# Optimization experiments

Hardware: AMD Instinct MI355X
Metric: run time of the kernel (lower is better)

The kernel has to match this reference:

```python
import jax, jax.numpy as jnp
import numpy as np

B, N, K, H, F_IN = 16, 2048, 8, 128, 4  # graphs, nodes/graph, knn k, hidden, input feats


def _lin(key, fi, fo):
    s = 1.0 / np.sqrt(fi)
    kw, kb = jax.random.split(key)
    W = jax.random.uniform(kw, (fi, fo), jnp.float32, -s, s)
    b = jax.random.uniform(kb, (fo,), jnp.float32, -s, s)
    return W, b


def setup_inputs() -> dict:
    key = jax.random.key(0)
    ks = jax.random.split(key, 10)
    x = jax.random.normal(ks[0], (B * N, F_IN), jnp.float32)
    edge_index = jax.random.randint(ks[1], (2, B * N * K), 0, B * N, jnp.int64)  # unused by forward
    batch = jnp.repeat(jnp.arange(B, dtype=jnp.int64), N)
    W_enc, b_enc = _lin(ks[2], F_IN, H)
    W1a, b1a = _lin(ks[3], 2 * H, H)
    W1b, b1b = _lin(ks[4], H, H)
    W2a, b2a = _lin(ks[5], 2 * H, H)
    W2b, b2b = _lin(ks[6], H, H)
    W5a, b5a = _lin(ks[7], 2 * H, H)
    W5b, b5b = _lin(ks[8], H, 1)
    return dict(x=x, edge_index=edge_index, batch=batch,
                W_enc=W_enc, b_enc=b_enc,
                W1a=W1a, b1a=b1a, W1b=W1b, b1b=b1b,
                W2a=W2a, b2a=b2a, W2b=W2b, b2b=b2b,
                W5a=W5a, b5a=b5a, W5b=W5b, b5b=b5b)


def _knn(xb):
    # xb: [N, H] -> [N, K] indices of k nearest neighbors (self included, as in torch_cluster.knn)
    sq = jnp.sum(xb * xb, axis=-1)
    d = sq[:, None] + sq[None, :] - 2.0 * (xb @ xb.T)  # squared distances [N, N]
    return jax.lax.top_k(-d, K)[1]


def _edge_conv(x, Wa, ba, Wb, bb):
    # DynamicEdgeConv: rebuild kNN on current features, message = MLP([x_i, x_j - x_i]), max-aggregate.
    idx = jax.vmap(_knn)(x)                                   # [B, N, K]
    xj = jax.vmap(lambda xb, ib: xb[ib])(x, idx)              # [B, N, K, Hin]
    xi = jnp.broadcast_to(x[:, :, None, :], xj.shape)
    e = jnp.concatenate([xi, xj - xi], axis=-1)               # [B, N, K, 2*Hin]
    h = jax.nn.relu(e @ Wa + ba)                              # MLP applies ReLU after each Linear
    h = jax.nn.relu(h @ Wb + bb)
    return jnp.max(h, axis=2)                                 # max aggregation over neighbors


def reference(x, edge_index, batch, W_enc, b_enc,
              W1a, b1a, W1b, b1b, W2a, b2a, W2b, b2b, W5a, b5a, W5b, b5b):
    # batch is contiguous equal-size graphs -> reshape; edge_index is ignored by the original forward.
    h = x.reshape(B, N, F_IN) @ W_enc + b_enc
    h = jax.nn.relu(_edge_conv(h, W1a, b1a, W1b, b1b))
    h = jax.nn.relu(_edge_conv(h, W2a, b2a, W2b, b2b))
    out = jax.nn.sigmoid(_edge_conv(h, W5a, b5a, W5b, b5b))   # note: last MLP layer also has ReLU
    return out.reshape(B * N, 1)
```

## Files before the change

### kernel.cpp

```cpp
#include <hip/hip_runtime.h>
#include <hip/hip_bf16.h>
#include <math.h>

#define BGR 16
#define NPG 2048
#define HD  128
#define KNN 8
#define NTOT (BGR*NPG)

using bf16x8 = __attribute__((ext_vector_type(8))) short;
using f32x4  = __attribute__((ext_vector_type(4))) float;
using f32x16 = __attribute__((ext_vector_type(16))) float;

typedef __attribute__((address_space(3))) unsigned int lds_uint;
typedef const __attribute__((address_space(1))) unsigned int glob_uint;
#define GLOAD_LDS16(g, l) __builtin_amdgcn_global_load_lds((glob_uint*)(g), (lds_uint*)(l), 16, 0, 0)

__device__ inline unsigned short bf16rn(float f) {
    unsigned u = __float_as_uint(f);
    unsigned r = (u + 0x7FFFu + ((u >> 16) & 1u)) >> 16;
    return (unsigned short)r;
}
__device__ inline float bf16tof(unsigned short h) {
    return __uint_as_float(((unsigned)h) << 16);
}

__global__ __launch_bounds__(256) void enc_split(const float* __restrict__ x,
                                                 const float* __restrict__ W,
                                                 const float* __restrict__ bias,
                                                 unsigned short* __restrict__ hs,
                                                 float* __restrict__ sqg)
{
    const size_t plane = (size_t)NTOT * HD;
    int node = (blockIdx.x * 256 + threadIdx.x) >> 6;
    int lane = threadIdx.x & 63;
    float4 xv = *(const float4*)(x + (size_t)node * 4);
    float v0 = bias[lane], v1 = bias[lane + 64];
    const float* xf = (const float*)&xv;
#pragma unroll
    for (int f = 0; f < 4; ++f) {
        v0 = fmaf(xf[f], W[f * 128 + lane], v0);
        v1 = fmaf(xf[f], W[f * 128 + lane + 64], v1);
    }
    float s = fmaf(v0, v0, v1 * v1);
#pragma unroll
    for (int off = 32; off >= 1; off >>= 1)
        s += __shfl_xor(s, off);
    if (lane == 0) sqg[node] = s;
#pragma unroll
    for (int q = 0; q < 2; ++q) {
        float v = q ? v1 : v0;
        int   d = lane + q * 64;
        unsigned short b1 = bf16rn(v);  float r1 = v - bf16tof(b1);
        unsigned short b2 = bf16rn(r1);
        size_t base = (size_t)node * HD + d;
        hs[base]         = b1;
        hs[base + plane] = b2;
    }
}

__global__ __launch_bounds__(256) void prep_wcat(const float* __restrict__ Wa,
                                                 unsigned short* __restrict__ Wt)
{
    int gid = blockIdx.x * 256 + threadIdx.x;
    int k = gid >> 8, n = gid & 255;
    float w;
    if (n < 128) w = Wa[(128 + k) * 128 + n];
    else { int nn = n - 128; w = Wa[k * 128 + nn] - Wa[(128 + k) * 128 + nn]; }
    unsigned short b1 = bf16rn(w);  float r1 = w - bf16tof(b1);
    unsigned short b2 = bf16rn(r1);
    int cs = n >> 5, h = (n >> 4) & 1, c = n & 15, kc = k >> 5, kg = (k >> 3) & 3, e = k & 7;
    size_t off = (size_t)cs * 12288 + kc * 1024 + h * 512 + kg * 128 + c * 8 + e;
    Wt[off] = b1; Wt[off + 4096] = b2;
}

__global__ __launch_bounds__(256) void prep_wb(const float* __restrict__ Wb,
                                               unsigned short* __restrict__ Wt)
{
    int gid = blockIdx.x * 256 + threadIdx.x;
    int k = gid >> 7, n = gid & 127;
    float w = Wb[k * 128 + n];
    unsigned short b1 = bf16rn(w);  float r1 = w - bf16tof(b1);
    unsigned short b2 = bf16rn(r1);
    int cs = n >> 5, h = (n >> 4) & 1, c = n & 15, kc = k >> 5, kg = (k >> 3) & 3, e = k & 7;
    size_t off = (size_t)cs * 12288 + kc * 1024 + h * 512 + kg * 128 + c * 8 + e;
    Wt[off] = b1; Wt[off + 4096] = b2;
}

#define THREEPASS(B00,B01,B10,B11) \
    acc0 = __builtin_amdgcn_mfma_f32_16x16x32_bf16(A0[kc], B00, acc0, 0, 0, 0); \
    acc1 = __builtin_amdgcn_mfma_f32_16x16x32_bf16(A0[kc], B01, acc1, 0, 0, 0); \
    acc0 = __builtin_amdgcn_mfma_f32_16x16x32_bf16(A1[kc], B00, acc0, 0, 0, 0); \
    acc1 = __builtin_amdgcn_mfma_f32_16x16x32_bf16(A1[kc], B01, acc1, 0, 0, 0); \
    acc0 = __builtin_amdgcn_mfma_f32_16x16x32_bf16(A0[kc], B10, acc0, 0, 0, 0); \
    acc1 = __builtin_amdgcn_mfma_f32_16x16x32_bf16(A0[kc], B11, acc1, 0, 0, 0);

#define SELECT(PACC, PS) { \
    const unsigned lidbase = (unsigned)((PS) << 4); \
    _Pragma("unroll") \
    for (int grp = 0; grp < 4; ++grp) { \
        f32x4 sq4 = *(const f32x4*)(sqs + (PS) * 32 + grp * 8 + kh * 4); \
        _Pragma("unroll") \
        for (int e = 0; e < 4; ++e) { \
            float dp = (sqi + sq4[e]) + (PACC)[grp * 4 + e]; \
            unsigned ku = (__float_as_uint(dp) & 0xFFFFFF00u) \
                        | (lidbase + (unsigned)(grp * 4 + e)); \
            float kk = __uint_as_float(ku); \
            bd[7] = __builtin_amdgcn_fmed3f(bd[6], kk, bd[7]); \
            bd[6] = __builtin_amdgcn_fmed3f(bd[5], kk, bd[6]); \
            bd[5] = __builtin_amdgcn_fmed3f(bd[4], kk, bd[5]); \
            bd[4] = __builtin_amdgcn_fmed3f(bd[3], kk, bd[4]); \
            bd[3] = __builtin_amdgcn_fmed3f(bd[2], kk, bd[3]); \
            bd[2] = __builtin_amdgcn_fmed3f(bd[1], kk, bd[2]); \
            bd[1] = __builtin_amdgcn_fmed3f(bd[0], kk, bd[1]); \
            bd[0] = fminf(bd[0], kk); \
        } \
    } }

__global__ __launch_bounds__(256, 3) void knn_mfma(const unsigned short* __restrict__ hs,
                                                   const float* __restrict__ sqg,
                                                   float* __restrict__ cand_d,
                                                   int* __restrict__ cand_i)
{
    __shared__ ulong2 ldsraw[2176];
    char* ldsc = (char*)ldsraw;
    float* sqs = (float*)(ldsc + 32768);

    const size_t plane = (size_t)NTOT * HD;
    const int t = threadIdx.x;
    const int b = blockIdx.x;
    const int slot = b >> 3;
    const int g  = (b & 7) | ((slot & 1) << 3);
    const int rb = (slot >> 1) & 15;
    const int cs = (slot >> 5) & 3;
    const int gbase = g * NPG;
    const int cbase = cs * 512;
    const int wv = t >> 6, lane = t & 63;
    const int rl = lane & 31, kh = lane >> 5;
    const int myrow = rb * 128 + wv * 32 + rl;

    sqs[t]       = sqg[gbase + cbase + t];
    sqs[t + 256] = sqg[gbase + cbase + 256 + t];

    bf16x8 RB[2][8];
    {
        const unsigned short* rrow = hs + (size_t)(gbase + myrow) * HD + kh * 8;
#pragma unroll
        for (int p = 0; p < 2; ++p)
#pragma unroll
            for (int kch = 0; kch < 8; ++kch) {
                bf16x8 v = *(const bf16x8*)(rrow + (size_t)p * plane + kch * 16);
                unsigned* u = (unsigned*)&v;
#pragma unroll
                for (int w = 0; w < 4; ++w)
                    u[w] = (u[w] + 0x00800080u) ^ 0x80008000u;
                RB[p][kch] = v;
            }
    }
    const float sqi = sqg[gbase + myrow];

    const unsigned short* sb = hs + (size_t)(gbase + cbase + (t & 31)) * HD
                             + (t >> 6) * 16 + ((t >> 5) & 1) * 8;
    char* ldsw = ldsc + wv * 1024;

#pragma unroll
    for (int i = 0; i < 4; ++i)
        GLOAD_LDS16(sb + (size_t)(i >> 1) * plane + (i & 1) * 64, ldsw + i * 4096);
    __syncthreads();

    const float INF = __uint_as_float(0x7F800000u);
    float bd[8];
#pragma unroll
    for (int s = 0; s < 8; ++s) bd[s] = INF;

    f32x16 pacc;
    int cur = 0;
    for (int s = 0; s < 16; ++s) {
        if (s < 15) {
            const unsigned short* sbn = sb + (size_t)(s + 1) * 32 * HD;
#pragma unroll
            for (int i = 0; i < 4; ++i)
                GLOAD_LDS16(sbn + (size_t)(i >> 1) * plane + (i & 1) * 64,
                            ldsw + (cur ^ 1) * 16384 + i * 4096);
        }
        const char* pstep = ldsc + cur * 16384 + lane * 16;
        f32x16 acc = {0.f,0.f,0.f,0.f,0.f,0.f,0.f,0.f,0.f,0.f,0.f,0.f,0.f,0.f,0.f,0.f};
        __builtin_amdgcn_s_setprio(1);
#pragma unroll
        for (int kch = 0; kch < 8; ++kch) {
            bf16x8 c0 = *(const bf16x8*)(pstep + kch * 1024);
            bf16x8 c1 = *(const bf16x8*)(pstep + 8192 + kch * 1024);
            acc = __builtin_amdgcn_mfma_f32_32x32x16_bf16(c0, RB[0][kch], acc, 0, 0, 0);
            acc = __builtin_amdgcn_mfma_f32_32x32x16_bf16(c1, RB[0][kch], acc, 0, 0, 0);
            acc = __builtin_amdgcn_mfma_f32_32x32x16_bf16(c0, RB[1][kch], acc, 0, 0, 0);
        }
        __builtin_amdgcn_s_setprio(0);
        if (s > 0) SELECT(pacc, s - 1)
        pacc = acc;
        __syncthreads();
        cur ^= 1;
    }
    SELECT(pacc, 15)

    const size_t ob = (size_t)(gbase + myrow) * 64 + cs * 16 + kh * 8;
#pragma unroll
    for (int sel = 0; sel < 8; ++sel) {
        unsigned u = __float_as_uint(bd[sel]);
        unsigned lid = u & 255u;
        int j = cbase + (int)(lid >> 4) * 32 + (int)((lid >> 2) & 3u) * 8
              + kh * 4 + (int)(lid & 3u);
        cand_d[ob + sel] = bd[sel];
        cand_i[ob + sel] = gbase + j;
    }
}

__global__ __launch_bounds__(256) void knn_merge(const float* __restrict__ cand_d,
                                                 const int* __restrict__ cand_i,
                                                 int* __restrict__ nbr)
{
    const int t = threadIdx.x;
    const int row = blockIdx.x * 32 + (t >> 3);
    const int run = t & 7;
    const float* pd = cand_d + (size_t)row * 64 + run * 8;
    const int*   pi = cand_i + (size_t)row * 64 + run * 8;
    float d[8]; int ix[8];
#pragma unroll
    for (int k = 0; k < 8; ++k) { d[k] = pd[k]; ix[k] = pi[k]; }
    const float INF = __uint_as_float(0x7F800000u);
    int* op = nbr + (size_t)row * KNN;
    float hd = d[0]; int hi = ix[0];
#pragma unroll
    for (int sel = 0; sel < 8; ++sel) {
        float md = hd; int mi = hi;
#pragma unroll
        for (int m = 1; m < 8; m <<= 1) {
            float od = __shfl_xor(md, m, 8);
            int   oi = __shfl_xor(mi, m, 8);
            bool tk = (od < md) || (od == md && oi < mi);
            md = tk ? od : md; mi = tk ? oi : mi;
        }
        if (run == sel) op[sel] = mi;
        bool win = (hd == md) && (hi == mi);
        if (win) {
            d[0]=d[1]; ix[0]=ix[1]; d[1]=d[2]; ix[1]=ix[2];
            d[2]=d[3]; ix[2]=ix[3]; d[3]=d[4]; ix[3]=ix[4];
            d[4]=d[5]; ix[4]=ix[5]; d[5]=d[6]; ix[5]=ix[6];
            d[6]=d[7]; ix[6]=ix[7]; d[7]=INF;  ix[7]=0x7fffffff;
        }
        hd = d[0]; hi = ix[0];
    }
}

__global__ __launch_bounds__(256) void node_gemm(const unsigned short* __restrict__ hs,
                                                 const unsigned short* __restrict__ Wt,
                                                 const float* __restrict__ ba,
                                                 float* __restrict__ P,
                                                 float* __restrict__ D)
{
    __shared__ char lds[32768];
    const size_t plane = (size_t)NTOT * HD;
    const int t = threadIdx.x, wv = t >> 6, lane = t & 63;
    const int lrow = lane & 15, kg = lane >> 4;
    const int nodebase = blockIdx.x * 64 + wv * 16;

    const unsigned short* arow = hs + (size_t)(nodebase + lrow) * HD + kg * 8;
    bf16x8 A0[4], A1[4];
#pragma unroll
    for (int kc = 0; kc < 4; ++kc) {
        A0[kc] = *(const bf16x8*)(arow + kc * 32);
        A1[kc] = *(const bf16x8*)(arow + plane + kc * 32);
    }

    char* ldsw = lds + wv * 1024;
    const unsigned short* wsrc = Wt + t * 8;
#pragma unroll
    for (int i = 0; i < 4; ++i)
        GLOAD_LDS16(wsrc + i * 2048, ldsw + i * 4096);
    __syncthreads();

    int cur = 0;
    for (int cs = 0; cs < 8; ++cs) {
        if (cs < 7) {
#pragma unroll
            for (int i = 0; i < 4; ++i)
                GLOAD_LDS16(wsrc + (size_t)(cs + 1) * 12288 + i * 2048,
                            ldsw + (cur ^ 1) * 16384 + i * 4096);
        }
        const char* pb = lds + cur * 16384 + kg * 256 + lrow * 16;
        f32x4 acc0 = {0.f,0.f,0.f,0.f};
        f32x4 acc1 = {0.f,0.f,0.f,0.f};
#pragma unroll
        for (int kc = 0; kc < 4; ++kc) {
            const char* pk = pb + kc * 2048;
            bf16x8 b00 = *(const bf16x8*)(pk);
            bf16x8 b01 = *(const bf16x8*)(pk + 1024);
            bf16x8 b10 = *(const bf16x8*)(pk + 8192);
            bf16x8 b11 = *(const bf16x8*)(pk + 9216);
            THREEPASS(b00, b01, b10, b11)
        }
        int n0 = cs * 32 + lrow;
        if (cs < 4) {
#pragma unroll
            for (int r = 0; r < 4; ++r) {
                size_t row = (size_t)(nodebase + kg * 4 + r) * HD;
                P[row + n0]      = acc0[r];
                P[row + n0 + 16] = acc1[r];
            }
        } else {
            float ba0 = ba[n0 - 128], ba1 = ba[n0 - 112];
#pragma unroll
            for (int r = 0; r < 4; ++r) {
                size_t row = (size_t)(nodebase + kg * 4 + r) * HD;
                D[row + n0 - 128] = acc0[r] + ba0;
                D[row + n0 - 112] = acc1[r] + ba1;
            }
        }
        __syncthreads();
        cur ^= 1;
    }
}

template<bool FINAL>
__global__ __launch_bounds__(256) void edge_mlp(const float* __restrict__ P,
                                                const float* __restrict__ D,
                                                const int* __restrict__ nbr,
                                                const unsigned short* __restrict__ Wbt,
                                                const float* __restrict__ bb,
                                                const float* __restrict__ w5,
                                                unsigned short* __restrict__ hsout,
                                                float* __restrict__ sqgout,
                                                float* __restrict__ out)
{
    __shared__ char lds[32768];
    const size_t plane = (size_t)NTOT * HD;
    const int t = threadIdx.x, wv = t >> 6, lane = t & 63;
    const int lrow = lane & 15, kg = lane >> 4;
    const int nodeA = blockIdx.x * 8 + wv * 2;
    const int i_node = nodeA + (lrow >> 3);
    const int j = nbr[(size_t)i_node * KNN + (lrow & 7)];

    const float* dp = D + (size_t)i_node * HD + kg * 8;
    const float* pp = P + (size_t)j * HD + kg * 8;

    bf16x8 A0[4], A1[4];
    float sdot = 0.f;
#pragma unroll
    for (int kc = 0; kc < 4; ++kc) {
        float4 d0 = *(const float4*)(dp + kc * 32);
        float4 d1 = *(const float4*)(dp + kc * 32 + 4);
        float4 p0 = *(const float4*)(pp + kc * 32);
        float4 p1 = *(const float4*)(pp + kc * 32 + 4);
        float v[8];
        v[0]=fmaxf(d0.x+p0.x,0.f); v[1]=fmaxf(d0.y+p0.y,0.f);
        v[2]=fmaxf(d0.z+p0.z,0.f); v[3]=fmaxf(d0.w+p0.w,0.f);
        v[4]=fmaxf(d1.x+p1.x,0.f); v[5]=fmaxf(d1.y+p1.y,0.f);
        v[6]=fmaxf(d1.z+p1.z,0.f); v[7]=fmaxf(d1.w+p1.w,0.f);
        if (FINAL) {
#pragma unroll
            for (int e = 0; e < 8; ++e)
                sdot = fmaf(v[e], w5[kc * 32 + kg * 8 + e], sdot);
        } else {
#pragma unroll
            for (int e = 0; e < 8; ++e) {
                unsigned short b1 = bf16rn(v[e]); float r1 = v[e] - bf16tof(b1);
                unsigned short b2 = bf16rn(r1);
                A0[kc][e] = (short)b1; A1[kc][e] = (short)b2;
            }
        }
    }

    if (!FINAL) {
        char* ldsw = lds + wv * 1024;
        const unsigned short* wsrc = Wbt + t * 8;
#pragma unroll
        for (int i = 0; i < 4; ++i)
            GLOAD_LDS16(wsrc + i * 2048, ldsw + i * 4096);
        __syncthreads();

        const int mynode = nodeA + (kg >> 1);
        const bool writer = (kg & 1) == 0;
        float sqacc = 0.f;

        int cur = 0;
        for (int cs = 0; cs < 4; ++cs) {
            if (cs < 3) {
#pragma unroll
                for (int i = 0; i < 4; ++i)
                    GLOAD_LDS16(wsrc + (size_t)(cs + 1) * 12288 + i * 2048,
                                ldsw + (cur ^ 1) * 16384 + i * 4096);
            }
            const char* pb = lds + cur * 16384 + kg * 256 + lrow * 16;
            f32x4 acc0 = {0.f,0.f,0.f,0.f};
            f32x4 acc1 = {0.f,0.f,0.f,0.f};
#pragma unroll
            for (int kc = 0; kc < 4; ++kc) {
                const char* pk = pb + kc * 2048;
                bf16x8 b00 = *(const bf16x8*)(pk);
                bf16x8 b01 = *(const bf16x8*)(pk + 1024);
                bf16x8 b10 = *(const bf16x8*)(pk + 8192);
                bf16x8 b11 = *(const bf16x8*)(pk + 9216);
                THREEPASS(b00, b01, b10, b11)
            }
            float bb0 = bb[cs * 32 + lrow];
            float bb1 = bb[cs * 32 + 16 + lrow];
            float m0 = fmaxf(fmaxf(acc0[0], acc0[1]), fmaxf(acc0[2], acc0[3]));
            float m1 = fmaxf(fmaxf(acc1[0], acc1[1]), fmaxf(acc1[2], acc1[3]));
            m0 = fmaxf(m0 + bb0, 0.f);
            m1 = fmaxf(m1 + bb1, 0.f);
            m0 = fmaxf(m0, __shfl_xor(m0, 16));
            m1 = fmaxf(m1, __shfl_xor(m1, 16));
            if (writer) {
                sqacc = fmaf(m0, m0, fmaf(m1, m1, sqacc));
                size_t base = (size_t)mynode * HD + cs * 32 + lrow;
                unsigned short c1 = bf16rn(m0); float r1 = m0 - bf16tof(c1);
                unsigned short c2 = bf16rn(r1);
                hsout[base]         = c1;
                hsout[base + plane] = c2;
                unsigned short e1 = bf16rn(m1); float s1 = m1 - bf16tof(e1);
                unsigned short e2 = bf16rn(s1);
                hsout[base + 16]         = e1;
                hsout[base + 16 + plane] = e2;
            }
            __syncthreads();
            cur ^= 1;
        }
        if (writer) {
#pragma unroll
            for (int m = 1; m < 16; m <<= 1)
                sqacc += __shfl_xor(sqacc, m, 16);
            if (lrow == 0) sqgout[mynode] = sqacc;
        }
    } else {
        sdot += __shfl_xor(sdot, 16);
        sdot += __shfl_xor(sdot, 32);
        float s = fmaxf(sdot + bb[0], 0.f);
#pragma unroll
        for (int m = 1; m < 8; m <<= 1)
            s = fmaxf(s, __shfl_xor(s, m));
        if (lane == 0) out[nodeA]     = 1.f / (1.f + expf(-s));
        if (lane == 8) out[nodeA + 1] = 1.f / (1.f + expf(-s));
    }
}

extern "C" void kernel_launch(void* const* d_in, const int* in_sizes, int n_in,
                              void* d_out, int out_size, void* d_ws, size_t ws_size,
                              hipStream_t stream) {
    const float* x     = (const float*)d_in[0];
    const float* W_enc = (const float*)d_in[3];
    const float* b_enc = (const float*)d_in[4];
    const float* W1a = (const float*)d_in[5];
    const float* b1a = (const float*)d_in[6];
    const float* W1b = (const float*)d_in[7];
    const float* b1b = (const float*)d_in[8];
    const float* W2a = (const float*)d_in[9];
    const float* b2a = (const float*)d_in[10];
    const float* W2b = (const float*)d_in[11];
    const float* b2b = (const float*)d_in[12];
    const float* W5a = (const float*)d_in[13];
    const float* b5a = (const float*)d_in[14];
    const float* W5b = (const float*)d_in[15];
    const float* b5b = (const float*)d_in[16];

    unsigned short* hs = (unsigned short*)d_ws;
    float* sqg  = (float*)(hs + (size_t)2*NTOT*HD);
    int*   idxb = (int*)(sqg + NTOT);
    float* Dbuf = (float*)(idxb + (size_t)NTOT*KNN);
    float* Pbuf = Dbuf + (size_t)NTOT*HD;
    unsigned short* Wt1  = (unsigned short*)(Pbuf + (size_t)NTOT*HD);
    unsigned short* Wt2  = Wt1 + 98304;
    unsigned short* Wt5  = Wt2 + 98304;
    unsigned short* Wbt1 = Wt5 + 98304;
    unsigned short* Wbt2 = Wbt1 + 49152;

    float* cd = Dbuf;
    int*   ci = (int*)(Dbuf + (size_t)NTOT*64);

    prep_wcat<<<128, 256, 0, stream>>>(W1a, Wt1);
    prep_wcat<<<128, 256, 0, stream>>>(W2a, Wt2);
    prep_wcat<<<128, 256, 0, stream>>>(W5a, Wt5);
    prep_wb  <<< 64, 256, 0, stream>>>(W1b, Wbt1);
    prep_wb  <<< 64, 256, 0, stream>>>(W2b, Wbt2);

    enc_split<<<NTOT/4, 256, 0, stream>>>(x, W_enc, b_enc, hs, sqg);

    knn_mfma   <<<1024, 256, 0, stream>>>(hs, sqg, cd, ci);
    knn_merge  <<<NTOT/32, 256, 0, stream>>>(cd, ci, idxb);
    node_gemm  <<<NTOT/64, 256, 0, stream>>>(hs, Wt1, b1a, Pbuf, Dbuf);
    edge_mlp<false><<<NTOT/8, 256, 0, stream>>>(Pbuf, Dbuf, idxb, Wbt1, b1b, nullptr, hs, sqg, nullptr);

    knn_mfma   <<<1024, 256, 0, stream>>>(hs, sqg, cd, ci);
    knn_merge  <<<NTOT/32, 256, 0, stream>>>(cd, ci, idxb);
    node_gemm  <<<NTOT/64, 256, 0, stream>>>(hs, Wt2, b2a, Pbuf, Dbuf);
    edge_mlp<false><<<NTOT/8, 256, 0, stream>>>(Pbuf, Dbuf, idxb, Wbt2, b2b, nullptr, hs, sqg, nullptr);

    knn_mfma   <<<1024, 256, 0, stream>>>(hs, sqg, cd, ci);
    knn_merge  <<<NTOT/32, 256, 0, stream>>>(cd, ci, idxb);
    node_gemm  <<<NTOT/64, 256, 0, stream>>>(hs, Wt5, b5a, Pbuf, Dbuf);
    edge_mlp<true><<<NTOT/8, 256, 0, stream>>>(Pbuf, Dbuf, idxb, nullptr, b5b, W5b, nullptr, nullptr, (float*)d_out);
}
```

Measured before the change: 372.1 us.

## Fuse setup kernels, merge kNN with node GEMM, fold merge into edge MLP

Combines the encoder and all weight-prep kernels into one launch. Runs the node GEMM as extra blocks in the same launch as the kNN MFMA kernel, since both read the same features. Moves the top-k candidate merge into the start of the edge MLP kernel, with the neighbour list kept in LDS, and issues the weight prefetch earlier. The kNN loop is unrolled by two with separate accumulators so SELECT overlaps the next MFMA step. Together this cuts six launches per layer pass plus the idx buffer round trip, at the cost of more complex blocks and a separate workspace for candidates.

```diff
diff --git a/kernel.cpp b/kernel.cpp
--- a/kernel.cpp
+++ b/kernel.cpp
@@ -25,44 +25,10 @@
     return __uint_as_float(((unsigned)h) << 16);
 }
 
-__global__ __launch_bounds__(256) void enc_split(const float* __restrict__ x,
-                                                 const float* __restrict__ W,
-                                                 const float* __restrict__ bias,
-                                                 unsigned short* __restrict__ hs,
-                                                 float* __restrict__ sqg)
+__device__ inline void wcat_body(const float* __restrict__ Wa,
+                                 unsigned short* __restrict__ Wt, int lb, int t)
 {
-    const size_t plane = (size_t)NTOT * HD;
-    int node = (blockIdx.x * 256 + threadIdx.x) >> 6;
-    int lane = threadIdx.x & 63;
-    float4 xv = *(const float4*)(x + (size_t)node * 4);
-    float v0 = bias[lane], v1 = bias[lane + 64];
-    const float* xf = (const float*)&xv;
-#pragma unroll
-    for (int f = 0; f < 4; ++f) {
-        v0 = fmaf(xf[f], W[f * 128 + lane], v0);
-        v1 = fmaf(xf[f], W[f * 128 + lane + 64], v1);
-    }
-    float s = fmaf(v0, v0, v1 * v1);
-#pragma unroll
-    for (int off = 32; off >= 1; off >>= 1)
-        s += __shfl_xor(s, off);
-    if (lane == 0) sqg[node] = s;
-#pragma unroll
-    for (int q = 0; q < 2; ++q) {
-        float v = q ? v1 : v0;
-        int   d = lane + q * 64;
-        unsigned short b1 = bf16rn(v);  float r1 = v - bf16tof(b1);
-        unsigned short b2 = bf16rn(r1);
-        size_t base = (size_t)node * HD + d;
-        hs[base]         = b1;
-        hs[base + plane] = b2;
-    }
-}
-
-__global__ __launch_bounds__(256) void prep_wcat(const float* __restrict__ Wa,
-                                                 unsigned short* __restrict__ Wt)
-{
-    int gid = blockIdx.x * 256 + threadIdx.x;
+    int gid = lb * 256 + t;
     int k = gid >> 8, n = gid & 255;
     float w;
     if (n < 128) w = Wa[(128 + k) * 128 + n];
@@ -74,10 +40,10 @@
     Wt[off] = b1; Wt[off + 4096] = b2;
 }
 
-__global__ __launch_bounds__(256) void prep_wb(const float* __restrict__ Wb,
-                                               unsigned short* __restrict__ Wt)
+__device__ inline void wb_body(const float* __restrict__ Wb,
+                               unsigned short* __restrict__ Wt, int lb, int t)
 {
-    int gid = blockIdx.x * 256 + threadIdx.x;
+    int gid = lb * 256 + t;
     int k = gid >> 7, n = gid & 127;
     float w = Wb[k * 128 + n];
     unsigned short b1 = bf16rn(w);  float r1 = w - bf16tof(b1);
@@ -85,6 +51,58 @@
     int cs = n >> 5, h = (n >> 4) & 1, c = n & 15, kc = k >> 5, kg = (k >> 3) & 3, e = k & 7;
     size_t off = (size_t)cs * 12288 + kc * 1024 + h * 512 + kg * 128 + c * 8 + e;
     Wt[off] = b1; Wt[off + 4096] = b2;
+}
+
+__global__ __launch_bounds__(256) void setup_all(const float* __restrict__ x,
+                                                 const float* __restrict__ We,
+                                                 const float* __restrict__ be,
+                                                 unsigned short* __restrict__ hs,
+                                                 float* __restrict__ sqg,
+                                                 const float* __restrict__ W1a,
+                                                 const float* __restrict__ W2a,
+                                                 const float* __restrict__ W5a,
+                                                 const float* __restrict__ W1b,
+                                                 const float* __restrict__ W2b,
+                                                 unsigned short* __restrict__ Wt1,
+                                                 unsigned short* __restrict__ Wt2,
+                                                 unsigned short* __restrict__ Wt5,
+                                                 unsigned short* __restrict__ Wbt1,
+                                                 unsigned short* __restrict__ Wbt2)
+{
+    const int bb = blockIdx.x, t = threadIdx.x;
+    if (bb < 8192) {
+        const size_t plane = (size_t)NTOT * HD;
+        int node = (bb * 256 + t) >> 6;
+        int lane = t & 63;
+        float4 xv = *(const float4*)(x + (size_t)node * 4);
+        float v0 = be[lane], v1 = be[lane + 64];
+        const float* xf = (const float*)&xv;
+#pragma unroll
+        for (int f = 0; f < 4; ++f) {
+            v0 = fmaf(xf[f], We[f * 128 + lane], v0);
+            v1 = fmaf(xf[f], We[f * 128 + lane + 64], v1);
+        }
+        float s = fmaf(v0, v0, v1 * v1);
+#pragma unroll
+        for (int off = 32; off >= 1; off >>= 1)
+            s += __shfl_xor(s, off);
+        if (lane == 0) sqg[node] = s;
+#pragma unroll
+        for (int q = 0; q < 2; ++q) {
+            float v = q ? v1 : v0;
+            int   d = lane + q * 64;
+            unsigned short b1 = bf16rn(v);  float r1 = v - bf16tof(b1);
+            unsigned short b2 = bf16rn(r1);
+            size_t base = (size_t)node * HD + d;
+            hs[base]         = b1;
+            hs[base + plane] = b2;
+        }
+    }
+    else if (bb < 8320) wcat_body(W1a, Wt1, bb - 8192, t);
+    else if (bb < 8448) wcat_body(W2a, Wt2, bb - 8320, t);
+    else if (bb < 8576) wcat_body(W5a, Wt5, bb - 8448, t);
+    else if (bb < 8640) wb_body(W1b, Wbt1, bb - 8576, t);
+    else                wb_body(W2b, Wbt2, bb - 8640, t);
 }
 
 #define THREEPASS(B00,B01,B10,B11) \
@@ -117,25 +135,105 @@
         } \
     } }
 
-__global__ __launch_bounds__(256, 3) void knn_mfma(const unsigned short* __restrict__ hs,
+#define KNN_MFMA_STEP(ACC) { \
+    ACC = (f32x16){0.f,0.f,0.f,0.f,0.f,0.f,0.f,0.f,0.f,0.f,0.f,0.f,0.f,0.f,0.f,0.f}; \
+    const char* pstep = ldsc + cur * 16384 + lane * 16; \
+    __builtin_amdgcn_s_setprio(1); \
+    _Pragma("unroll") \
+    for (int kch = 0; kch < 8; ++kch) { \
+        bf16x8 c0 = *(const bf16x8*)(pstep + kch * 1024); \
+        bf16x8 c1 = *(const bf16x8*)(pstep + 8192 + kch * 1024); \
+        ACC = __builtin_amdgcn_mfma_f32_32x32x16_bf16(c0, RB[0][kch], ACC, 0, 0, 0); \
+        ACC = __builtin_amdgcn_mfma_f32_32x32x16_bf16(c1, RB[0][kch], ACC, 0, 0, 0); \
+        ACC = __builtin_amdgcn_mfma_f32_32x32x16_bf16(c0, RB[1][kch], ACC, 0, 0, 0); \
+    } \
+    __builtin_amdgcn_s_setprio(0); }
+
+__global__ __launch_bounds__(256, 3) void knn_node(const unsigned short* __restrict__ hs,
                                                    const float* __restrict__ sqg,
+                                                   const unsigned short* __restrict__ Wt,
+                                                   const float* __restrict__ ba,
+                                                   float* __restrict__ P,
+                                                   float* __restrict__ D,
                                                    float* __restrict__ cand_d,
                                                    int* __restrict__ cand_i)
 {
     __shared__ ulong2 ldsraw[2176];
     char* ldsc = (char*)ldsraw;
-    float* sqs = (float*)(ldsc + 32768);
-
     const size_t plane = (size_t)NTOT * HD;
     const int t = threadIdx.x;
-    const int b = blockIdx.x;
+    const int wv = t >> 6, lane = t & 63;
+
+    if (blockIdx.x < 512) {
+        const int lrow = lane & 15, kg = lane >> 4;
+        const int nodebase = blockIdx.x * 64 + wv * 16;
+
+        const unsigned short* arow = hs + (size_t)(nodebase + lrow) * HD + kg * 8;
+        bf16x8 A0[4], A1[4];
+#pragma unroll
+        for (int kc = 0; kc < 4; ++kc) {
+            A0[kc] = *(const bf16x8*)(arow + kc * 32);
+            A1[kc] = *(const bf16x8*)(arow + plane + kc * 32);
+        }
+
+        char* ldsw = ldsc + wv * 1024;
+        const unsigned short* wsrc = Wt + t * 8;
+#pragma unroll
+        for (int i = 0; i < 4; ++i)
+            GLOAD_LDS16(wsrc + i * 2048, ldsw + i * 4096);
+        __syncthreads();
+
+        int cur = 0;
+        for (int cs = 0; cs < 8; ++cs) {
+            if (cs < 7) {
+#pragma unroll
+                for (int i = 0; i < 4; ++i)
+                    GLOAD_LDS16(wsrc + (size_t)(cs + 1) * 12288 + i * 2048,
+                                ldsc + (cur ^ 1) * 16384 + wv * 1024 + i * 4096);
+            }
+            const char* pb = ldsc + cur * 16384 + kg * 256 + lrow * 16;
+            f32x4 acc0 = {0.f,0.f,0.f,0.f};
+            f32x4 acc1 = {0.f,0.f,0.f,0.f};
+#pragma unroll
+            for (int kc = 0; kc < 4; ++kc) {
+                const char* pk = pb + kc * 2048;
+                bf16x8 b00 = *(const bf16x8*)(pk);
+                bf16x8 b01 = *(const bf16x8*)(pk + 1024);
+                bf16x8 b10 = *(const bf16x8*)(pk + 8192);
+                bf16x8 b11 = *(const bf16x8*)(pk + 9216);
+                THREEPASS(b00, b01, b10, b11)
+            }
+            int n0 = cs * 32 + lrow;
+            if (cs < 4) {
+#pragma unroll
+                for (int r = 0; r < 4; ++r) {
+                    size_t row = (size_t)(nodebase + kg * 4 + r) * HD;
+                    P[row + n0]      = acc0[r];
+                    P[row + n0 + 16] = acc1[r];
+                }
+            } else {
+                float ba0 = ba[n0 - 128], ba1 = ba[n0 - 112];
+#pragma unroll
+                for (int r = 0; r < 4; ++r) {
+                    size_t row = (size_t)(nodebase + kg * 4 + r) * HD;
+                    D[row + n0 - 128] = acc0[r] + ba0;
+                    D[row + n0 - 112] = acc1[r] + ba1;
+                }
+            }
+            __syncthreads();
+            cur ^= 1;
+        }
+        return;
+    }
+
+    float* sqs = (float*)(ldsc + 32768);
+    const int b = blockIdx.x - 512;
     const int slot = b >> 3;
     const int g  = (b & 7) | ((slot & 1) << 3);
     const int rb = (slot >> 1) & 15;
     const int cs = (slot >> 5) & 3;
     const int gbase = g * NPG;
     const int cbase = cs * 512;
-    const int wv = t >> 6, lane = t & 63;
     const int rl = lane & 31, kh = lane >> 5;
     const int myrow = rb * 128 + wv * 32 + rl;
 
@@ -173,34 +271,36 @@
 #pragma unroll
     for (int s = 0; s < 8; ++s) bd[s] = INF;
 
-    f32x16 pacc;
+    f32x16 accA, accB;
     int cur = 0;
-    for (int s = 0; s < 16; ++s) {
-        if (s < 15) {
-            const unsigned short* sbn = sb + (size_t)(s + 1) * 32 * HD;
+    for (int sp = 0; sp < 8; ++sp) {
+        const int s0 = sp * 2;
+        {
+            const unsigned short* sbn = sb + (size_t)(s0 + 1) * 32 * HD;
 #pragma unroll
             for (int i = 0; i < 4; ++i)
                 GLOAD_LDS16(sbn + (size_t)(i >> 1) * plane + (i & 1) * 64,
-                            ldsw + (cur ^ 1) * 16384 + i * 4096);
-        }
-        const char* pstep = ldsc + cur * 16384 + lane * 16;
-        f32x16 acc = {0.f,0.f,0.f,0.f,0.f,0.f,0.f,0.f,0.f,0.f,0.f,0.f,0.f,0.f,0.f,0.f};
-        __builtin_amdgcn_s_setprio(1);
-#pragma unroll
-        for (int kch = 0; kch < 8; ++kch) {
-            bf16x8 c0 = *(const bf16x8*)(pstep + kch * 1024);
-            bf16x8 c1 = *(const bf16x8*)(pstep + 8192 + kch * 1024);
-            acc = __builtin_amdgcn_mfma_f32_32x32x16_bf16(c0, RB[0][kch], acc, 0, 0, 0);
-            acc = __builtin_amdgcn_mfma_f32_32x32x16_bf16(c1, RB[0][kch], acc, 0, 0, 0);
-            acc = __builtin_amdgcn_mfma_f32_32x32x16_bf16(c0, RB[1][kch], acc, 0, 0, 0);
-        }
-        __builtin_amdgcn_s_setprio(0);
-        if (s > 0) SELECT(pacc, s - 1)
-        pacc = acc;
-        __syncthreads();
-        cur ^= 1;
-    }
-    SELECT(pacc, 15)
+                            ldsc + (cur ^ 1) * 16384 + wv * 1024 + i * 4096);
+            KNN_MFMA_STEP(accA)
+            if (sp > 0) SELECT(accB, s0 - 1)
+            __syncthreads();
+            cur ^= 1;
+        }
+        {
+            if (sp < 7) {
+                const unsigned short* sbn = sb + (size_t)(s0 + 2) * 32 * HD;
+#pragma unroll
+                for (int i = 0; i < 4; ++i)
+                    GLOAD_LDS16(sbn + (size_t)(i >> 1) * plane + (i & 1) * 64,
+                                ldsc + (cur ^ 1) * 16384 + wv * 1024 + i * 4096);
+            }
+            KNN_MFMA_STEP(accB)
+            SELECT(accA, s0)
+            __syncthreads();
+            cur ^= 1;
+        }
+    }
+    SELECT(accB, 15)
 
     const size_t ob = (size_t)(gbase + myrow) * 64 + cs * 16 + kh * 8;
 #pragma unroll
@@ -214,116 +314,11 @@
     }
 }
 
-__global__ __launch_bounds__(256) void knn_merge(const float* __restrict__ cand_d,
-                                                 const int* __restrict__ cand_i,
-                                                 int* __restrict__ nbr)
-{
-    const int t = threadIdx.x;
-    const int row = blockIdx.x * 32 + (t >> 3);
-    const int run = t & 7;
-    const float* pd = cand_d + (size_t)row * 64 + run * 8;
-    const int*   pi = cand_i + (size_t)row * 64 + run * 8;
-    float d[8]; int ix[8];
-#pragma unroll
-    for (int k = 0; k < 8; ++k) { d[k] = pd[k]; ix[k] = pi[k]; }
-    const float INF = __uint_as_float(0x7F800000u);
-    int* op = nbr + (size_t)row * KNN;
-    float hd = d[0]; int hi = ix[0];
-#pragma unroll
-    for (int sel = 0; sel < 8; ++sel) {
-        float md = hd; int mi = hi;
-#pragma unroll
-        for (int m = 1; m < 8; m <<= 1) {
-            float od = __shfl_xor(md, m, 8);
-            int   oi = __shfl_xor(mi, m, 8);
-            bool tk = (od < md) || (od == md && oi < mi);
-            md = tk ? od : md; mi = tk ? oi : mi;
-        }
-        if (run == sel) op[sel] = mi;
-        bool win = (hd == md) && (hi == mi);
-        if (win) {
-            d[0]=d[1]; ix[0]=ix[1]; d[1]=d[2]; ix[1]=ix[2];
-            d[2]=d[3]; ix[2]=ix[3]; d[3]=d[4]; ix[3]=ix[4];
-            d[4]=d[5]; ix[4]=ix[5]; d[5]=d[6]; ix[5]=ix[6];
-            d[6]=d[7]; ix[6]=ix[7]; d[7]=INF;  ix[7]=0x7fffffff;
-        }
-        hd = d[0]; hi = ix[0];
-    }
-}
-
-__global__ __launch_bounds__(256) void node_gemm(const unsigned short* __restrict__ hs,
-                                                 const unsigned short* __restrict__ Wt,
-                                                 const float* __restrict__ ba,
-                                                 float* __restrict__ P,
-                                                 float* __restrict__ D)
-{
-    __shared__ char lds[32768];
-    const size_t plane = (size_t)NTOT * HD;
-    const int t = threadIdx.x, wv = t >> 6, lane = t & 63;
-    const int lrow = lane & 15, kg = lane >> 4;
-    const int nodebase = blockIdx.x * 64 + wv * 16;
-
-    const unsigned short* arow = hs + (size_t)(nodebase + lrow) * HD + kg * 8;
-    bf16x8 A0[4], A1[4];
-#pragma unroll
-    for (int kc = 0; kc < 4; ++kc) {
-        A0[kc] = *(const bf16x8*)(arow + kc * 32);
-        A1[kc] = *(const bf16x8*)(arow + plane + kc * 32);
-    }
-
-    char* ldsw = lds + wv * 1024;
-    const unsigned short* wsrc = Wt + t * 8;
-#pragma unroll
-    for (int i = 0; i < 4; ++i)
-        GLOAD_LDS16(wsrc + i * 2048, ldsw + i * 4096);
-    __syncthreads();
-
-    int cur = 0;
-    for (int cs = 0; cs < 8; ++cs) {
-        if (cs < 7) {
-#pragma unroll
-            for (int i = 0; i < 4; ++i)
-                GLOAD_LDS16(wsrc + (size_t)(cs + 1) * 12288 + i * 2048,
-                            ldsw + (cur ^ 1) * 16384 + i * 4096);
-        }
-        const char* pb = lds + cur * 16384 + kg * 256 + lrow * 16;
-        f32x4 acc0 = {0.f,0.f,0.f,0.f};
-        f32x4 acc1 = {0.f,0.f,0.f,0.f};
-#pragma unroll
-        for (int kc = 0; kc < 4; ++kc) {
-            const char* pk = pb + kc * 2048;
-            bf16x8 b00 = *(const bf16x8*)(pk);
-            bf16x8 b01 = *(const bf16x8*)(pk + 1024);
-            bf16x8 b10 = *(const bf16x8*)(pk + 8192);
-            bf16x8 b11 = *(const bf16x8*)(pk + 9216);
-            THREEPASS(b00, b01, b10, b11)
-        }
-        int n0 = cs * 32 + lrow;
-        if (cs < 4) {
-#pragma unroll
-            for (int r = 0; r < 4; ++r) {
-                size_t row = (size_t)(nodebase + kg * 4 + r) * HD;
-                P[row + n0]      = acc0[r];
-                P[row + n0 + 16] = acc1[r];
-            }
-        } else {
-            float ba0 = ba[n0 - 128], ba1 = ba[n0 - 112];
-#pragma unroll
-            for (int r = 0; r < 4; ++r) {
-                size_t row = (size_t)(nodebase + kg * 4 + r) * HD;
-                D[row + n0 - 128] = acc0[r] + ba0;
-                D[row + n0 - 112] = acc1[r] + ba1;
-            }
-        }
-        __syncthreads();
-        cur ^= 1;
-    }
-}
-
 template<bool FINAL>
 __global__ __launch_bounds__(256) void edge_mlp(const float* __restrict__ P,
                                                 const float* __restrict__ D,
-                                                const int* __restrict__ nbr,
+                                                const float* __restrict__ cand_d,
+                                                const int* __restrict__ cand_i,
                                                 const unsigned short* __restrict__ Wbt,
                                                 const float* __restrict__ bb,
                                                 const float* __restrict__ w5,
@@ -331,13 +326,59 @@
                                                 float* __restrict__ sqgout,
                                                 float* __restrict__ out)
 {
-    __shared__ char lds[32768];
+    __shared__ ulong2 ldsraw[2080];
+    char* lds = (char*)ldsraw;
+    int* nbrs = (int*)(lds + 32768);
     const size_t plane = (size_t)NTOT * HD;
     const int t = threadIdx.x, wv = t >> 6, lane = t & 63;
     const int lrow = lane & 15, kg = lane >> 4;
-    const int nodeA = blockIdx.x * 8 + wv * 2;
-    const int i_node = nodeA + (lrow >> 3);
-    const int j = nbr[(size_t)i_node * KNN + (lrow & 7)];
+    const int node0 = blockIdx.x * 8;
+    const int nodeA = node0 + wv * 2;
+
+    char* ldsw = lds + wv * 1024;
+    const unsigned short* wsrc = Wbt + t * 8;
+    if (!FINAL) {
+#pragma unroll
+        for (int i = 0; i < 4; ++i)
+            GLOAD_LDS16(wsrc + i * 2048, ldsw + i * 4096);
+    }
+
+    if (t < 64) {
+        const int row = node0 + (t >> 3);
+        const int run = t & 7;
+        const float* pd = cand_d + (size_t)row * 64 + run * 8;
+        const int*   pi = cand_i + (size_t)row * 64 + run * 8;
+        float d[8]; int ix[8];
+#pragma unroll
+        for (int k = 0; k < 8; ++k) { d[k] = pd[k]; ix[k] = pi[k]; }
+        const float INF = __uint_as_float(0x7F800000u);
+        float hd = d[0]; int hi = ix[0];
+#pragma unroll
+        for (int sel = 0; sel < 8; ++sel) {
+            float md = hd; int mi = hi;
+#pragma unroll
+            for (int m = 1; m < 8; m <<= 1) {
+                float od = __shfl_xor(md, m, 8);
+                int   oi = __shfl_xor(mi, m, 8);
+                bool tk = (od < md) || (od == md && oi < mi);
+                md = tk ? od : md; mi = tk ? oi : mi;
+            }
+            if (run == sel) nbrs[(t >> 3) * 8 + sel] = mi;
+            bool win = (hd == md) && (hi == mi);
+            if (win) {
+                d[0]=d[1]; ix[0]=ix[1]; d[1]=d[2]; ix[1]=ix[2];
+                d[2]=d[3]; ix[2]=ix[3]; d[3]=d[4]; ix[3]=ix[4];
+                d[4]=d[5]; ix[4]=ix[5]; d[5]=d[6]; ix[5]=ix[6];
+                d[6]=d[7]; ix[6]=ix[7]; d[7]=INF;  ix[7]=0x7fffffff;
+            }
+            hd = d[0]; hi = ix[0];
+        }
+    }
+    __syncthreads();
+
+    const int i_local = wv * 2 + (lrow >> 3);
+    const int i_node = node0 + i_local;
+    const int j = nbrs[i_local * 8 + (lrow & 7)];
 
     const float* dp = D + (size_t)i_node * HD + kg * 8;
     const float* pp = P + (size_t)j * HD + kg * 8;
@@ -370,13 +411,6 @@
     }
 
     if (!FINAL) {
-        char* ldsw = lds + wv * 1024;
-        const unsigned short* wsrc = Wbt + t * 8;
-#pragma unroll
-        for (int i = 0; i < 4; ++i)
-            GLOAD_LDS16(wsrc + i * 2048, ldsw + i * 4096);
-        __syncthreads();
-
         const int mynode = nodeA + (kg >> 1);
         const bool writer = (kg & 1) == 0;
         float sqacc = 0.f;
@@ -387,7 +421,7 @@
 #pragma unroll
                 for (int i = 0; i < 4; ++i)
                     GLOAD_LDS16(wsrc + (size_t)(cs + 1) * 12288 + i * 2048,
-                                ldsw + (cur ^ 1) * 16384 + i * 4096);
+                                lds + (cur ^ 1) * 16384 + wv * 1024 + i * 4096);
             }
             const char* pb = lds + cur * 16384 + kg * 256 + lrow * 16;
             f32x4 acc0 = {0.f,0.f,0.f,0.f};
@@ -463,8 +497,9 @@
 
     unsigned short* hs = (unsigned short*)d_ws;
     float* sqg  = (float*)(hs + (size_t)2*NTOT*HD);
-    int*   idxb = (int*)(sqg + NTOT);
-    float* Dbuf = (float*)(idxb + (size_t)NTOT*KNN);
+    float* cd   = sqg + NTOT;
+    int*   ci   = (int*)(cd + (size_t)NTOT*64);
+    float* Dbuf = (float*)(ci + (size_t)NTOT*64);
     float* Pbuf = Dbuf + (size_t)NTOT*HD;
     unsigned short* Wt1  = (unsigned short*)(Pbuf + (size_t)NTOT*HD);
     unsigned short* Wt2  = Wt1 + 98304;
@@ -472,29 +507,16 @@
     unsigned short* Wbt1 = Wt5 + 98304;
     unsigned short* Wbt2 = Wbt1 + 49152;
 
-    float* cd = Dbuf;
-    int*   ci = (int*)(Dbuf + (size_t)NTOT*64);
-
-    prep_wcat<<<128, 256, 0, stream>>>(W1a, Wt1);
-    prep_wcat<<<128, 256, 0, stream>>>(W2a, Wt2);
-    prep_wcat<<<128, 256, 0, stream>>>(W5a, Wt5);
-    prep_wb  <<< 64, 256, 0, stream>>>(W1b, Wbt1);
-    prep_wb  <<< 64, 256, 0, stream>>>(W2b, Wbt2);
-
-    enc_split<<<NTOT/4, 256, 0, stream>>>(x, W_enc, b_enc, hs, sqg);
-
-    knn_mfma   <<<1024, 256, 0, stream>>>(hs, sqg, cd, ci);
-    knn_merge  <<<NTOT/32, 256, 0, stream>>>(cd, ci, idxb);
-    node_gemm  <<<NTOT/64, 256, 0, stream>>>(hs, Wt1, b1a, Pbuf, Dbuf);
-    edge_mlp<false><<<NTOT/8, 256, 0, stream>>>(Pbuf, Dbuf, idxb, Wbt1, b1b, nullptr, hs, sqg, nullptr);
-
-    knn_mfma   <<<1024, 256, 0, stream>>>(hs, sqg, cd, ci);
-    knn_merge  <<<NTOT/32, 256, 0, stream>>>(cd, ci, idxb);
-    node_gemm  <<<NTOT/64, 256, 0, stream>>>(hs, Wt2, b2a, Pbuf, Dbuf);
-    edge_mlp<false><<<NTOT/8, 256, 0, stream>>>(Pbuf, Dbuf, idxb, Wbt2, b2b, nullptr, hs, sqg, nullptr);
-
-    knn_mfma   <<<1024, 256, 0, stream>>>(hs, sqg, cd, ci);
-    knn_merge  <<<NTOT/32, 256, 0, stream>>>(cd, ci, idxb);
-    node_gemm  <<<NTOT/64, 256, 0, stream>>>(hs, Wt5, b5a, Pbuf, Dbuf);
-    edge_mlp<true><<<NTOT/8, 256, 0, stream>>>(Pbuf, Dbuf, idxb, nullptr, b5b, W5b, nullptr, nullptr, (float*)d_out);
-}
+    setup_all<<<8704, 256, 0, stream>>>(x, W_enc, b_enc, hs, sqg,
+                                        W1a, W2a, W5a, W1b, W2b,
+                                        Wt1, Wt2, Wt5, Wbt1, Wbt2);
+
+    knn_node<<<1536, 256, 0, stream>>>(hs, sqg, Wt1, b1a, Pbuf, Dbuf, cd, ci);
+    edge_mlp<false><<<NTOT/8, 256, 0, stream>>>(Pbuf, Dbuf, cd, ci, Wbt1, b1b, nullptr, hs, sqg, nullptr);
+
+    knn_node<<<1536, 256, 0, stream>>>(hs, sqg, Wt2, b2a, Pbuf, Dbuf, cd, ci);
+    edge_mlp<false><<<NTOT/8, 256, 0, stream>>>(Pbuf, Dbuf, cd, ci, Wbt2, b2b, nullptr, hs, sqg, nullptr);
+
+    knn_node<<<1536, 256, 0, stream>>>(hs, sqg, Wt5, b5a, Pbuf, Dbuf, cd, ci);
+    edge_mlp<true><<<NTOT/8, 256, 0, stream>>>(Pbuf, Dbuf, cd, ci, nullptr, b5b, W5b, nullptr, nullptr, (float*)d_out);
+}
```

New measurement: 343.5 us. 7.7% less time.
